# Kernel optimization log

Hardware: AMD Instinct MI355X
Metric: run time of the kernel (lower is better)

The kernel has to match this reference:

```python
import jax, jax.numpy as jnp
import numpy as np

D_H = 128
N_RBF = 16
R_MIN = 0.0
R_MAX = float(np.sqrt(2.0))


def _rbf(r):
    # Gaussian RBF expansion: centers linspace(R_MIN, R_MAX, N_RBF),
    # width = center spacing, exp(-(r-mu)^2 / (2*width^2))
    centers = jnp.linspace(R_MIN, R_MAX, N_RBF, dtype=r.dtype)
    width = (R_MAX - R_MIN) / (N_RBF - 1)
    gamma = 1.0 / (2.0 * width * width)
    return jnp.exp(-gamma * (r[:, None] - centers[None, :]) ** 2)


def setup_inputs() -> dict:
    key = jax.random.key(0)
    ks = jax.random.split(key, 16)
    N, E = 50000, 800000
    h = jax.random.normal(ks[0], (N, D_H), dtype=jnp.float32)
    x = jax.random.uniform(ks[1], (N, 2), dtype=jnp.float32)
    edge_index = jax.random.randint(ks[2], (2, E), 0, N, dtype=jnp.int64)
    edge_weight = jax.random.uniform(ks[3], (E,), dtype=jnp.float32)

    def lin(k, fan_in, fan_out):
        s = 1.0 / np.sqrt(fan_in)
        kw, kb = jax.random.split(k)
        W = jax.random.uniform(kw, (fan_in, fan_out), minval=-s, maxval=s, dtype=jnp.float32)
        b = jax.random.uniform(kb, (fan_out,), minval=-s, maxval=s, dtype=jnp.float32)
        return W, b

    Wm1, bm1 = lin(ks[4], 2 * D_H + N_RBF, D_H)
    Wm2, bm2 = lin(ks[5], D_H, D_H)
    Wh1, bh1 = lin(ks[6], 2 * D_H, D_H)
    Wh2, bh2 = lin(ks[7], D_H, D_H)
    ln_g = jnp.ones((D_H,), dtype=jnp.float32)
    ln_b = jnp.zeros((D_H,), dtype=jnp.float32)
    return {"h": h, "x": x, "edge_index": edge_index, "edge_weight": edge_weight,
            "Wm1": Wm1, "bm1": bm1, "Wm2": Wm2, "bm2": bm2,
            "Wh1": Wh1, "bh1": bh1, "Wh2": Wh2, "bh2": bh2,
            "ln_g": ln_g, "ln_b": ln_b}


def reference(h, x, edge_index, edge_weight, Wm1, bm1, Wm2, bm2, Wh1, bh1, Wh2, bh2, ln_g, ln_b):
    N = h.shape[0]
    src = edge_index[0]
    dst = edge_index[1]
    # per-edge geometry
    dx = x[src, :2] - x[dst, :2]                      # [E,2]
    r = jnp.sqrt(jnp.sum(dx * dx, axis=-1) + 1e-8)    # [E]
    rbf = _rbf(r)                                     # [E,n_rbf]
    # message MLP: Linear -> SiLU -> Linear
    m_in = jnp.concatenate([h[src], h[dst], rbf], axis=-1)  # [E, 2*d_h+n_rbf]
    m = jax.nn.silu(m_in @ Wm1 + bm1) @ Wm2 + bm2            # [E, d_h]
    m = m * edge_weight[:, None]
    # scatter-sum aggregate into destination nodes
    agg = jax.ops.segment_sum(m, dst, num_segments=N)        # [N, d_h]
    # node update MLP
    u_in = jnp.concatenate([h, agg], axis=-1)                # [N, 2*d_h]
    h_up = jax.nn.silu(u_in @ Wh1 + bh1) @ Wh2 + bh2         # [N, d_h]
    # residual + LayerNorm
    z = h + h_up
    mu = jnp.mean(z, axis=-1, keepdims=True)
    var = jnp.var(z, axis=-1, keepdims=True)
    return (z - mu) / jnp.sqrt(var + 1e-5) * ln_g + ln_b
```

## Files before the change

kernel.cpp:

```cpp
#include <hip/hip_runtime.h>
#include <hip/hip_bf16.h>
#include <math.h>

#define DH 128
#define NRBF 16
#define EB 256
#define NTAB 1025
#define SEGCAP 32

typedef unsigned short ushort_t;
typedef __attribute__((ext_vector_type(8))) short short8;
typedef __attribute__((ext_vector_type(4))) float floatx4;

__device__ __forceinline__ float silu_f(float v) {
    return v / (1.f + __expf(-v));
}
__device__ __forceinline__ unsigned pk_bf16(float lo, float hi) {
    __hip_bfloat162 h = __float22bfloat162_rn(make_float2(lo, hi));
    union { __hip_bfloat162 h2; unsigned u; } cv;
    cv.h2 = h;
    return cv.u;
}
__device__ __forceinline__ ushort_t f2bf1(float f) {
    unsigned u = __float_as_uint(f);
    u += 0x7FFFu + ((u >> 16) & 1u);
    return (ushort_t)(u >> 16);
}
__device__ __forceinline__ float bflo(unsigned u) { return __uint_as_float(u << 16); }
__device__ __forceinline__ float bfhi(unsigned u) { return __uint_as_float(u & 0xffff0000u); }
__device__ __forceinline__ float bf2f(ushort_t u) { return __uint_as_float(((unsigned)u) << 16); }

__device__ __forceinline__ int detect64(const int* __restrict__ ei) {
    int z = 0;
#pragma unroll
    for (int i = 0; i < 8; ++i) z |= ei[2 * i + 1];
    return (z == 0) ? 1 : 0;
}
__device__ __forceinline__ int load_dst(const int* ei, int is64, int e, int E) {
    return is64 ? ei[2 * E + 2 * e] : ei[E + e];
}
__device__ __forceinline__ int load_src(const int* ei, int is64, int e, int E) {
    return is64 ? ei[2 * e] : ei[e];
}

__global__ __launch_bounds__(256) void k_hist_prep(
    const int* __restrict__ ei, int* __restrict__ counts, int E,
    const float* __restrict__ Wm1, const float* __restrict__ Wm2,
    const float* __restrict__ Wh1, const float* __restrict__ Wh2,
    ushort_t* __restrict__ Tbf, ushort_t* __restrict__ W2f,
    ushort_t* __restrict__ W1mf, ushort_t* __restrict__ W1hf,
    ushort_t* __restrict__ W2hf, int nb_hist)
{
    const int b = blockIdx.x, tid = threadIdx.x;
    if (b < nb_hist) {
        const int e = b * 256 + tid;
        if (e < E) {
            const int is64 = detect64(ei);
            atomicAdd(&counts[load_dst(ei, is64, e, E)], 1);
        }
        return;
    }
    int b2 = b - nb_hist;
    if (b2 < 257) {
        const int i = b2 * 4 + (tid >> 6);
        if (i < NTAB) {
            const float WIDTH = 0.09428090415820634f;
            const float GAMMA = 56.25f;
            const float DELTA = 1.4142135623730951f / 1024.0f;
            const float r = (float)i * DELTA;
            const int c0 = (tid & 63) * 2;
            float a0 = 0.f, a1 = 0.f;
#pragma unroll
            for (int q = 0; q < NRBF; ++q) {
                const float dr = r - (float)q * WIDTH;
                const float w = __expf(-GAMMA * dr * dr);
                a0 = fmaf(w, Wm1[(256 + q) * DH + c0], a0);
                a1 = fmaf(w, Wm1[(256 + q) * DH + c0 + 1], a1);
            }
            *(unsigned*)(Tbf + (size_t)i * DH + c0) = pk_bf16(a0, a1);
        }
        return;
    }
    b2 -= 257;
    if (b2 < 8) {
        const int u = b2 * 256 + tid;
        const int col = u & 127, kclg = u >> 7;
        const int lg = kclg & 3, kc = kclg >> 2;
        unsigned o[4];
#pragma unroll
        for (int j = 0; j < 2; ++j) {
            o[j]     = pk_bf16(Wm2[(kc * 32 + 4 * lg + 2 * j) * DH + col],
                               Wm2[(kc * 32 + 4 * lg + 2 * j + 1) * DH + col]);
            o[2 + j] = pk_bf16(Wm2[(kc * 32 + 16 + 4 * lg + 2 * j) * DH + col],
                               Wm2[(kc * 32 + 16 + 4 * lg + 2 * j + 1) * DH + col]);
        }
        *(uint4*)(W2f + 8 * u) = make_uint4(o[0], o[1], o[2], o[3]);
        return;
    }
    b2 -= 8;
    if (b2 < 16) {
        const int u = b2 * 256 + tid;
        const int c = u & 255, kclg = u >> 8;
        const int lg = kclg & 3, kc = kclg >> 2;
        const int base = (c < 128) ? 0 : 128;
        const int cc = c & 127;
        unsigned o[4];
#pragma unroll
        for (int j = 0; j < 2; ++j) {
            o[j]     = pk_bf16(Wm1[(base + kc * 32 + 4 * lg + 2 * j) * DH + cc],
                               Wm1[(base + kc * 32 + 4 * lg + 2 * j + 1) * DH + cc]);
            o[2 + j] = pk_bf16(Wm1[(base + kc * 32 + 16 + 4 * lg + 2 * j) * DH + cc],
                               Wm1[(base + kc * 32 + 16 + 4 * lg + 2 * j + 1) * DH + cc]);
        }
        *(uint4*)(W1mf + 8 * u) = make_uint4(o[0], o[1], o[2], o[3]);
        return;
    }
    b2 -= 16;
    if (b2 < 16) {
        const int u = b2 * 256 + tid;
        const int col = u & 127, kclg = u >> 7;
        const int lg = kclg & 3, kc = kclg >> 2;
        unsigned o[4];
#pragma unroll
        for (int j = 0; j < 2; ++j) {
            o[j]     = pk_bf16(Wh1[(kc * 32 + 4 * lg + 2 * j) * DH + col],
                               Wh1[(kc * 32 + 4 * lg + 2 * j + 1) * DH + col]);
            o[2 + j] = pk_bf16(Wh1[(kc * 32 + 16 + 4 * lg + 2 * j) * DH + col],
                               Wh1[(kc * 32 + 16 + 4 * lg + 2 * j + 1) * DH + col]);
        }
        *(uint4*)(W1hf + 8 * u) = make_uint4(o[0], o[1], o[2], o[3]);
        return;
    }
    b2 -= 16;
    {
        const int u = b2 * 256 + tid;
        const int col = u & 127, kclg = u >> 7;
        const int lg = kclg & 3, kc = kclg >> 2;
        unsigned o[4];
#pragma unroll
        for (int j = 0; j < 2; ++j) {
            o[j]     = pk_bf16(Wh2[(kc * 32 + 4 * lg + 2 * j) * DH + col],
                               Wh2[(kc * 32 + 4 * lg + 2 * j + 1) * DH + col]);
            o[2 + j] = pk_bf16(Wh2[(kc * 32 + 16 + 4 * lg + 2 * j) * DH + col],
                               Wh2[(kc * 32 + 16 + 4 * lg + 2 * j + 1) * DH + col]);
        }
        *(uint4*)(W2hf + 8 * u) = make_uint4(o[0], o[1], o[2], o[3]);
    }
}

__global__ __launch_bounds__(1024) void k_scan(const int* __restrict__ counts,
                                               int* __restrict__ cursor, int N) {
    __shared__ int wsum[16];
    __shared__ int sCarry;
    const int tid = threadIdx.x, lane = tid & 63, wid = tid >> 6;
    if (tid == 0) sCarry = 0;
    __syncthreads();
    for (int c0 = 0; c0 < N; c0 += 4096) {
        const int idx = c0 + tid * 4;
        int4 v = make_int4(0, 0, 0, 0);
        if (idx < N) v = *(const int4*)(counts + idx);
        const int t01 = v.x + v.y;
        const int t012 = t01 + v.z;
        const int tot = t012 + v.w;
        int incl = tot;
#pragma unroll
        for (int d = 1; d < 64; d <<= 1) {
            int t = __shfl_up(incl, d, 64);
            if (lane >= d) incl += t;
        }
        if (lane == 63) wsum[wid] = incl;
        __syncthreads();
        if (wid == 0) {
            int s = (lane < 16) ? wsum[lane] : 0;
#pragma unroll
            for (int d = 1; d < 16; d <<= 1) {
                int t = __shfl_up(s, d, 64);
                if (lane >= d) s += t;
            }
            if (lane < 16) wsum[lane] = s;
        }
        __syncthreads();
        const int ex = sCarry + (wid > 0 ? wsum[wid - 1] : 0) + incl - tot;
        if (idx + 3 < N) {
            *(int4*)(cursor + idx) = make_int4(ex, ex + v.x, ex + t01, ex + t012);
        } else if (idx < N) {
            cursor[idx] = ex;
            if (idx + 1 < N) cursor[idx + 1] = ex + v.x;
            if (idx + 2 < N) cursor[idx + 2] = ex + t01;
        }
        __syncthreads();
        if (tid == 0) sCarry += wsum[15];
        __syncthreads();
    }
}

__global__ __launch_bounds__(256) void k_scatter_pre(
    const int* __restrict__ ei, const float* __restrict__ ew, const float* __restrict__ x,
    int* __restrict__ cursor, uint2* __restrict__ spk, int* __restrict__ dstS,
    int E, int pack,
    const float* __restrict__ h, const float* __restrict__ bm1,
    const ushort_t* __restrict__ W1mf,
    ushort_t* __restrict__ Abf, ushort_t* __restrict__ Bbf, int N, int nb_scat)
{
    const int tid = threadIdx.x;

    if ((int)blockIdx.x < nb_scat) {
        const int e = blockIdx.x * 256 + tid;
        if (e < E) {
            const int is64 = detect64(ei);
            const int s = load_src(ei, is64, e, E);
            const int d = load_dst(ei, is64, e, E);
            const int pos = atomicAdd(&cursor[d], 1);
            unsigned x0 = (unsigned)s;
            if (pack) {
                const float2 xs = *(const float2*)(x + 2 * s);
                const float2 xd = *(const float2*)(x + 2 * d);
                const float dxv = xs.x - xd.x, dyv = xs.y - xd.y;
                const float r = sqrtf(dxv * dxv + dyv * dyv + 1e-8f);
                int ti = (int)(r * 724.0773439350246f + 0.5f);
                ti = min(ti, NTAB - 1);
                x0 |= ((unsigned)ti << 16);
            }
            spk[pos] = make_uint2(x0, __float_as_uint(ew[e]));
            dstS[pos] = d;
        }
        return;
    }

    __shared__ __align__(16) ushort_t sIn[64 * DH];
    const int nblk = ((int)blockIdx.x - nb_scat) * 64;

    {
        const int row = tid >> 2, q = tid & 3;
        const int gn = nblk + row;
        const float4* ps = (const float4*)(h + (size_t)gn * DH + 32 * q);
        uint4* rowp = (uint4*)(sIn + row * DH);
        const int swz = row & 7;
#pragma unroll
        for (int i = 0; i < 4; ++i) {
            uint4 o = make_uint4(0, 0, 0, 0);
            if (gn < N) {
                const float4 g0 = ps[2 * i], g1 = ps[2 * i + 1];
                o.x = pk_bf16(g0.x, g0.y); o.y = pk_bf16(g0.z, g0.w);
                o.z = pk_bf16(g1.x, g1.y); o.w = pk_bf16(g1.z, g1.w);
            }
            rowp[(4 * q + i) ^ swz] = o;
        }
    }
    __syncthreads();

    const int lane = tid & 63, wv = tid >> 6;
    const int lr = lane & 15, lg = lane >> 4;
    const int m0l = wv * 16;

    union FragU { unsigned u[4]; short8 s8; };
    floatx4 acc[16];
#pragma unroll
    for (int ni = 0; ni < 16; ++ni) acc[ni] = (floatx4){0.f, 0.f, 0.f, 0.f};

#pragma unroll
    for (int kc = 0; kc < 4; ++kc) {
        const int b1 = 64 * kc + 8 * lg;
        const int b2 = b1 + 32;
        const int row = m0l + lr;
        const char* rbase = (const char*)(sIn + row * DH);
        const int swz = (row & 7) << 4;
        FragU af;
        const uint2 lo = *(const uint2*)(rbase + ((b1 & ~15) ^ swz) + (b1 & 15));
        const uint2 hi = *(const uint2*)(rbase + ((b2 & ~15) ^ swz) + (b2 & 15));
        af.u[0] = lo.x; af.u[1] = lo.y; af.u[2] = hi.x; af.u[3] = hi.y;
        const ushort_t* wbase = W1mf + ((size_t)(kc * 4 + lg) * 256 + lr) * 8;
        __builtin_amdgcn_s_setprio(1);
#pragma unroll
        for (int ni = 0; ni < 16; ++ni) {
            const short8 bf = *(const short8*)(wbase + ni * 128);
            acc[ni] = __builtin_amdgcn_mfma_f32_16x16x32_bf16(af.s8, bf, acc[ni], 0, 0, 0);
        }
        __builtin_amdgcn_s_setprio(0);
    }

    float bm1v[8];
#pragma unroll
    for (int ni = 0; ni < 8; ++ni) bm1v[ni] = bm1[ni * 16 + lr];
#pragma unroll
    for (int r = 0; r < 4; ++r) {
        const int gn = nblk + m0l + 4 * lg + r;
        if (gn < N) {
#pragma unroll
            for (int ni = 0; ni < 8; ++ni)
                Abf[(size_t)gn * DH + ni * 16 + lr] = f2bf1(acc[ni][r] + bm1v[ni]);
#pragma unroll
            for (int ni = 8; ni < 16; ++ni)
                Bbf[(size_t)gn * DH + (ni - 8) * 16 + lr] = f2bf1(acc[ni][r]);
        }
    }
}

__global__ __launch_bounds__(256, 2) void k_edge(
    const float* __restrict__ x, const int* __restrict__ ei, const float* __restrict__ ew,
    const uint2* __restrict__ spk, const int* __restrict__ dstS,
    const ushort_t* __restrict__ W2f, const float* __restrict__ bm2,
    const ushort_t* __restrict__ Abf, const ushort_t* __restrict__ Bbf,
    const ushort_t* __restrict__ Tbf, float* __restrict__ agg,
    int sorted, int pack, int N, int E)
{
    __shared__ __align__(16) ushort_t sHid[4][16 * DH];
    __shared__ __align__(16) float ldsAgg[SEGCAP][DH];
    __shared__ int   sSrc[EB];
    __shared__ int   sDst[EB];
    __shared__ int   sLid[EB];
    __shared__ int   sTi[EB];
    __shared__ float sEw[EB];
    __shared__ int   sSegStart[SEGCAP];
    __shared__ int   sNseg;
    __shared__ int   sWtot[4];

    const int tid  = threadIdx.x;
    const int lane = tid & 63;
    const int wv   = tid >> 6;
    const int lr   = lane & 15;
    const int lg   = lane >> 4;
    const int e4   = lane >> 2;
    const int q    = lane & 3;
    const int wbase = wv * 64;

    const int nwg = gridDim.x;
    const int xcd = blockIdx.x & 7;
    const int cidx = blockIdx.x >> 3;
    const int qch = nwg >> 3, rch = nwg & 7;
    const int bid = (xcd < rch) ? (xcd * (qch + 1) + cidx)
                                : (rch * (qch + 1) + (xcd - rch) * qch + cidx);
    const int e0 = bid * EB;

    const int fast = sorted && pack;

    union FragU { unsigned u[4]; short8 s8; };

    FragU bfr[4][8];
#pragma unroll
    for (int kc = 0; kc < 4; ++kc)
#pragma unroll
        for (int ni = 0; ni < 8; ++ni)
            *(uint4*)bfr[kc][ni].u =
                *(const uint4*)(W2f + ((size_t)(kc * 4 + lg) * 128 + ni * 16 + lr) * 8);

    {
        const float4 z = make_float4(0.f, 0.f, 0.f, 0.f);
        float4* za = (float4*)&ldsAgg[0][0];
#pragma unroll
        for (int i = 0; i < 4; ++i) za[tid + 256 * i] = z;
    }

    {
        const int slot = e0 + tid;
        int s = 0, d = 0, ti = 0;
        float w = 0.f;
        if (slot < E) {
            if (sorted) {
                const uint2 v = spk[slot];
                d = dstS[slot];
                w = __uint_as_float(v.y);
                if (pack) { s = (int)(v.x & 0xFFFFu); ti = (int)(v.x >> 16); }
                else {
                    s = (int)v.x;
                    const float2 xs = *(const float2*)(x + 2 * s);
                    const float2 xd = *(const float2*)(x + 2 * d);
                    const float dxv = xs.x - xd.x, dyv = xs.y - xd.y;
                    const float r = sqrtf(dxv * dxv + dyv * dyv + 1e-8f);
                    ti = min((int)(r * 724.0773439350246f + 0.5f), NTAB - 1);
                }
            } else {
                const int is64 = detect64(ei);
                s = load_src(ei, is64, slot, E);
                d = load_dst(ei, is64, slot, E);
                w = ew[slot];
                const float2 xs = *(const float2*)(x + 2 * s);
                const float2 xd = *(const float2*)(x + 2 * d);
                const float dxv = xs.x - xd.x, dyv = xs.y - xd.y;
                const float r = sqrtf(dxv * dxv + dyv * dyv + 1e-8f);
                ti = min((int)(r * 724.0773439350246f + 0.5f), NTAB - 1);
            }
        } else {
            d = sorted ? dstS[E - 1] : load_dst(ei, detect64(ei), E - 1, E);
        }
        sSrc[tid] = s; sDst[tid] = d; sEw[tid] = w; sTi[tid] = ti;
    }
    __syncthreads();

    {
        const int bflag = (tid > 0) && (sDst[tid] != sDst[tid - 1]);
        int incl = bflag;
#pragma unroll
        for (int dd = 1; dd < 64; dd <<= 1) {
            int t = __shfl_up(incl, dd, 64);
            if (lane >= dd) incl += t;
        }
        if (lane == 63) sWtot[wv] = incl;
        __syncthreads();
        int off = 0;
#pragma unroll
        for (int wq = 0; wq < 3; ++wq)
            if (wq < wv) off += sWtot[wq];
        incl += off;
        sLid[tid] = incl;
        if ((bflag || tid == 0) && incl < SEGCAP) sSegStart[incl] = tid;
        if (tid == EB - 1) sNseg = incl + 1;
    }
    __syncthreads();

    float bc8[8];
#pragma unroll
    for (int ni = 0; ni < 8; ++ni) bc8[ni] = bm2[ni * 16 + lr];

    ushort_t* slice = &sHid[wv][0];
    floatx4 acc[8];

#pragma unroll
    for (int st = 0; st < 4; ++st) {
        const int sb = wbase + st * 16;

        const int le = sb + e4;
        const int s  = sSrc[le];
        const int d  = sDst[le];
        const int ti = sTi[le];
        const uint4* pA = (const uint4*)(Abf + (size_t)s * DH + 32 * q);
        const uint4* pB = (const uint4*)(Bbf + (size_t)d * DH + 32 * q);
        const uint4* pT = (const uint4*)(Tbf + (size_t)ti * DH + 32 * q);
        uint4 av[4], bv[4], tv[4];
#pragma unroll
        for (int i = 0; i < 4; ++i) { av[i] = pA[i]; bv[i] = pB[i]; tv[i] = pT[i]; }

        {
            uint4* rowp = (uint4*)(slice + e4 * DH);
            const int swzw = e4 & 7;
#pragma unroll
            for (int i = 0; i < 4; ++i) {
                const uint4 a = av[i]; const uint4 b = bv[i]; const uint4 t = tv[i];
                const float v0 = bflo(a.x) + bflo(b.x) + bflo(t.x);
                const float v1 = bfhi(a.x) + bfhi(b.x) + bfhi(t.x);
                const float v2 = bflo(a.y) + bflo(b.y) + bflo(t.y);
                const float v3 = bfhi(a.y) + bfhi(b.y) + bfhi(t.y);
                const float v4 = bflo(a.z) + bflo(b.z) + bflo(t.z);
                const float v5 = bfhi(a.z) + bfhi(b.z) + bfhi(t.z);
                const float v6 = bflo(a.w) + bflo(b.w) + bflo(t.w);
                const float v7 = bfhi(a.w) + bfhi(b.w) + bfhi(t.w);
                uint4 pk;
                pk.x = pk_bf16(silu_f(v0), silu_f(v1));
                pk.y = pk_bf16(silu_f(v2), silu_f(v3));
                pk.z = pk_bf16(silu_f(v4), silu_f(v5));
                pk.w = pk_bf16(silu_f(v6), silu_f(v7));
                rowp[(4 * q + i) ^ swzw] = pk;
            }
        }

#pragma unroll
        for (int ni = 0; ni < 8; ++ni) acc[ni] = (floatx4){0.f, 0.f, 0.f, 0.f};
#pragma unroll
        for (int kc = 0; kc < 4; ++kc) {
            const int bo1 = 64 * kc + 8 * lg;
            const int bo2 = bo1 + 32;
            const char* rbase = (const char*)(slice + lr * DH);
            const int swzf = (lr & 7) << 4;
            FragU af;
            const uint2 lo = *(const uint2*)(rbase + ((bo1 & ~15) ^ swzf) + (bo1 & 15));
            const uint2 hi = *(const uint2*)(rbase + ((bo2 & ~15) ^ swzf) + (bo2 & 15));
            af.u[0] = lo.x; af.u[1] = lo.y; af.u[2] = hi.x; af.u[3] = hi.y;
            __builtin_amdgcn_s_setprio(1);
#pragma unroll
            for (int ni = 0; ni < 8; ++ni)
                acc[ni] = __builtin_amdgcn_mfma_f32_16x16x32_bf16(af.s8, bfr[kc][ni].s8, acc[ni], 0, 0, 0);
            __builtin_amdgcn_s_setprio(0);
        }

        {
            const int sbg = sb + 4 * lg;
            int lid4[4]; float ew4[4];
#pragma unroll
            for (int r = 0; r < 4; ++r) { lid4[r] = sLid[sbg + r]; ew4[r] = sEw[sbg + r]; }
#pragma unroll
            for (int ni = 0; ni < 8; ++ni) {
                const int col = ni * 16 + lr;
                const float bc = bc8[ni];
                int cur = lid4[0], curSlot = sbg;
                float avv = (acc[ni][0] + bc) * ew4[0];
#pragma unroll
                for (int r = 1; r < 4; ++r) {
                    const int l2 = lid4[r];
                    const float v = (acc[ni][r] + bc) * ew4[r];
                    if (l2 == cur) avv += v;
                    else {
                        if (cur < SEGCAP) atomicAdd(&ldsAgg[cur][col], avv);
                        else atomicAdd(agg + (size_t)sDst[curSlot] * DH + col, avv);
                        cur = l2; curSlot = sbg + r; avv = v;
                    }
                }
                if (cur < SEGCAP) atomicAdd(&ldsAgg[cur][col], avv);
                else atomicAdd(agg + (size_t)sDst[curSlot] * DH + col, avv);
            }
        }
    }

    __syncthreads();

    const int ns = sNseg;
    const int gmax = (ns < SEGCAP) ? ns : SEGCAP;
    for (int idx = tid; idx < (gmax << 7); idx += 256) {
        const int g = idx >> 7, col = idx & 127;
        const float v = ldsAgg[g][col];
        const int dst = sDst[sSegStart[g]];
        float* p = agg + (size_t)dst * DH + col;
        if (sorted && g > 0 && g < ns - 1) *p = v;
        else atomicAdd(p, v);
    }
}

__global__ __launch_bounds__(256) void k_node(
    const float* __restrict__ h, const float* __restrict__ agg,
    const ushort_t* __restrict__ W1hf, const float* __restrict__ bh1,
    const ushort_t* __restrict__ W2hf, const float* __restrict__ bh2,
    const float* __restrict__ ln_g, const float* __restrict__ ln_b,
    float* __restrict__ out, int N)
{
    __shared__ __align__(16) ushort_t sIn[64 * 256];
    __shared__ __align__(16) ushort_t sHid[64 * DH];
    const int tid = threadIdx.x;
    const int nblk = blockIdx.x * 64;

    {
        const int row = tid >> 2, q = tid & 3;
        const int gn = nblk + row;
        const float4* ps = (q < 2) ? (const float4*)(h + (size_t)gn * DH + 64 * q)
                                   : (const float4*)(agg + (size_t)gn * DH + 64 * (q - 2));
        uint4* rowp = (uint4*)(sIn + row * 256);
        const int swz = row & 7;
#pragma unroll
        for (int i = 0; i < 8; ++i) {
            uint4 o = make_uint4(0, 0, 0, 0);
            if (gn < N) {
                const float4 g0 = ps[2 * i], g1 = ps[2 * i + 1];
                o.x = pk_bf16(g0.x, g0.y); o.y = pk_bf16(g0.z, g0.w);
                o.z = pk_bf16(g1.x, g1.y); o.w = pk_bf16(g1.z, g1.w);
            }
            rowp[(8 * q + i) ^ swz] = o;
        }
    }
    __syncthreads();

    const int lane = tid & 63, wv = tid >> 6;
    const int lr = lane & 15, lg = lane >> 4;
    const int m0l = wv * 16;

    union FragU { unsigned u[4]; short8 s8; };

    floatx4 acc[8];
#pragma unroll
    for (int ni = 0; ni < 8; ++ni) acc[ni] = (floatx4){0.f, 0.f, 0.f, 0.f};

#pragma unroll
    for (int kc = 0; kc < 8; ++kc) {
        const int b1 = 64 * kc + 8 * lg;
        const int b2 = b1 + 32;
        const int row = m0l + lr;
        const char* rbase = (const char*)(sIn + row * 256);
        const int swz = (row & 7) << 4;
        FragU af;
        const uint2 lo = *(const uint2*)(rbase + ((b1 & ~15) ^ swz) + (b1 & 15));
        const uint2 hi = *(const uint2*)(rbase + ((b2 & ~15) ^ swz) + (b2 & 15));
        af.u[0] = lo.x; af.u[1] = lo.y; af.u[2] = hi.x; af.u[3] = hi.y;
        const ushort_t* wbase = W1hf + ((size_t)(kc * 4 + lg) * 128 + lr) * 8;
        __builtin_amdgcn_s_setprio(1);
#pragma unroll
        for (int ni = 0; ni < 8; ++ni) {
            const short8 bf = *(const short8*)(wbase + ni * 128);
            acc[ni] = __builtin_amdgcn_mfma_f32_16x16x32_bf16(af.s8, bf, acc[ni], 0, 0, 0);
        }
        __builtin_amdgcn_s_setprio(0);
    }

    {
        float bh1v[8];
#pragma unroll
        for (int ni = 0; ni < 8; ++ni) bh1v[ni] = bh1[ni * 16 + lr];
#pragma unroll
        for (int r = 0; r < 4; ++r) {
            const int row = m0l + 4 * lg + r;
            const int swz = row & 7;
            ushort_t* rp = sHid + row * DH;
#pragma unroll
            for (int ni = 0; ni < 8; ++ni) {
                const int col = ni * 16 + lr;
                rp[(((col >> 3) ^ swz) << 3) + (col & 7)] =
                    f2bf1(silu_f(acc[ni][r] + bh1v[ni]));
            }
        }
    }

    floatx4 acc2[8];
#pragma unroll
    for (int ni = 0; ni < 8; ++ni) acc2[ni] = (floatx4){0.f, 0.f, 0.f, 0.f};

#pragma unroll
    for (int kc = 0; kc < 4; ++kc) {
        const int b1 = 64 * kc + 8 * lg;
        const int b2 = b1 + 32;
        const int row = m0l + lr;
        const char* rbase = (const char*)(sHid + row * DH);
        const int swz = (row & 7) << 4;
        FragU af;
        const uint2 lo = *(const uint2*)(rbase + ((b1 & ~15) ^ swz) + (b1 & 15));
        const uint2 hi = *(const uint2*)(rbase + ((b2 & ~15) ^ swz) + (b2 & 15));
        af.u[0] = lo.x; af.u[1] = lo.y; af.u[2] = hi.x; af.u[3] = hi.y;
        const ushort_t* wbase = W2hf + ((size_t)(kc * 4 + lg) * 128 + lr) * 8;
        __builtin_amdgcn_s_setprio(1);
#pragma unroll
        for (int ni = 0; ni < 8; ++ni) {
            const short8 bf = *(const short8*)(wbase + ni * 128);
            acc2[ni] = __builtin_amdgcn_mfma_f32_16x16x32_bf16(af.s8, bf, acc2[ni], 0, 0, 0);
        }
        __builtin_amdgcn_s_setprio(0);
    }

    float gv[8], bv[8], b2v[8];
#pragma unroll
    for (int ni = 0; ni < 8; ++ni) {
        const int col = ni * 16 + lr;
        gv[ni] = ln_g[col]; bv[ni] = ln_b[col]; b2v[ni] = bh2[col];
    }
#pragma unroll
    for (int r = 0; r < 4; ++r) {
        const int row = m0l + 4 * lg + r;
        const int gn = nblk + row;
        const int swz = row & 7;
        float z[8];
        float s1 = 0.f, s2 = 0.f;
#pragma unroll
        for (int ni = 0; ni < 8; ++ni) {
            const int col = ni * 16 + lr;
            const float hv = bf2f(sIn[row * 256 + (((col >> 3) ^ swz) << 3) + (col & 7)]);
            z[ni] = acc2[ni][r] + b2v[ni] + hv;
            s1 += z[ni]; s2 += z[ni] * z[ni];
        }
#pragma unroll
        for (int m = 1; m < 16; m <<= 1) {
            s1 += __shfl_xor(s1, m, 64);
            s2 += __shfl_xor(s2, m, 64);
        }
        const float mean = s1 * (1.f / 128.f);
        const float var = s2 * (1.f / 128.f) - mean * mean;
        const float rstd = rsqrtf(var + 1e-5f);
        if (gn < N) {
#pragma unroll
            for (int ni = 0; ni < 8; ++ni) {
                const int col = ni * 16 + lr;
                out[(size_t)gn * DH + col] = (z[ni] - mean) * rstd * gv[ni] + bv[ni];
            }
        }
    }
}

extern "C" void kernel_launch(void* const* d_in, const int* in_sizes, int n_in,
                              void* d_out, int out_size, void* d_ws, size_t ws_size,
                              hipStream_t stream)
{
    (void)n_in; (void)out_size;
    const float* h   = (const float*)d_in[0];
    const float* x   = (const float*)d_in[1];
    const int*   ei  = (const int*)d_in[2];
    const float* ew  = (const float*)d_in[3];
    const float* Wm1 = (const float*)d_in[4];
    const float* bm1 = (const float*)d_in[5];
    const float* Wm2 = (const float*)d_in[6];
    const float* bm2 = (const float*)d_in[7];
    const float* Wh1 = (const float*)d_in[8];
    const float* bh1 = (const float*)d_in[9];
    const float* Wh2 = (const float*)d_in[10];
    const float* bh2 = (const float*)d_in[11];
    const float* lng = (const float*)d_in[12];
    const float* lnb = (const float*)d_in[13];
    float* out = (float*)d_out;

    const int N = in_sizes[0] / DH;
    const int E = in_sizes[3];

    float*    agg  = (float*)d_ws;
    ushort_t* Abf  = (ushort_t*)(agg + (size_t)N * DH);
    ushort_t* Bbf  = Abf + (size_t)N * DH;
    ushort_t* W2f  = Bbf + (size_t)N * DH;
    ushort_t* Tbf  = W2f + 16384;
    ushort_t* W1mf = Tbf + (size_t)NTAB * DH;
    ushort_t* W1hf = W1mf + 32768;
    ushort_t* W2hf = W1hf + 32768;
    int*   counts  = (int*)(W2hf + 16384);
    int*   cursor  = counts + N;
    uint2* spk     = (uint2*)(cursor + N);
    int*   dstS    = (int*)(spk + E);

    const size_t mand = (size_t)N * DH * 4 + (size_t)N * DH * 4
                      + ((size_t)16384 + (size_t)NTAB * DH + 32768 + 32768 + 16384) * 2;
    const size_t need = mand + (size_t)(2 * N) * 4 + (size_t)E * 12 + 64;
    const int use_sort = (ws_size >= need) ? 1 : 0;
    const int pack = use_sort && (N <= 65535);

    const int nb_hist = use_sort ? (E + 255) / 256 : 0;
    const int nb_prep = 257 + 8 + 16 + 16 + 8;
    const int nb_scat = nb_hist;
    const int nb_pre  = (N + 63) / 64;

    hipMemsetAsync(agg, 0, (size_t)N * DH * sizeof(float), stream);
    if (use_sort)
        hipMemsetAsync(counts, 0, (size_t)N * sizeof(int), stream);
    k_hist_prep<<<nb_hist + nb_prep, 256, 0, stream>>>(ei, counts, E, Wm1, Wm2, Wh1, Wh2,
                                                       Tbf, W2f, W1mf, W1hf, W2hf, nb_hist);
    if (use_sort)
        k_scan<<<1, 1024, 0, stream>>>(counts, cursor, N);
    k_scatter_pre<<<nb_scat + nb_pre, 256, 0, stream>>>(ei, ew, x, cursor, spk, dstS, E, pack,
                                                        h, bm1, W1mf, Abf, Bbf, N, nb_scat);
    k_edge<<<(E + EB - 1) / EB, 256, 0, stream>>>(x, ei, ew, spk, dstS,
                                                  W2f, bm2, Abf, Bbf, Tbf, agg,
                                                  use_sort, pack, N, E);
    k_node<<<(N + 63) / 64, 256, 0, stream>>>(h, agg, W1hf, bh1, W2hf, bh2, lng, lnb, out, N);
}
```

Measured before the change: 396.9 us.

## Prefetch all source-row gathers up front and stream W2 fragments from memory

The edge kernel now issues the Abf gathers for all four subtiles at the start and pins them in registers. This is meant to overlap gather latency with compute. To pay for those registers, it stops holding the W2 B-fragments in VGPRs and reloads them from global/L2 inside each MFMA loop. The sorted edge record is packed into one 16-byte uint4 that includes dst, replacing two separate arrays, and counts is placed next to agg so a single memset clears both. This trades higher L2 traffic for W2 and extra bytes per edge record against better latency hiding and fewer launches.

```diff
diff --git a/kernel.cpp b/kernel.cpp
--- a/kernel.cpp
+++ b/kernel.cpp
@@ -42,6 +42,8 @@
 __device__ __forceinline__ int load_src(const int* ei, int is64, int e, int E) {
     return is64 ? ei[2 * e] : ei[e];
 }
+
+#define PIN(u4) asm volatile("" :: "v"(u4.x), "v"(u4.y), "v"(u4.z), "v"(u4.w))
 
 __global__ __launch_bounds__(256) void k_hist_prep(
     const int* __restrict__ ei, int* __restrict__ counts, int E,
@@ -196,7 +198,7 @@
 
 __global__ __launch_bounds__(256) void k_scatter_pre(
     const int* __restrict__ ei, const float* __restrict__ ew, const float* __restrict__ x,
-    int* __restrict__ cursor, uint2* __restrict__ spk, int* __restrict__ dstS,
+    int* __restrict__ cursor, uint4* __restrict__ epk,
     int E, int pack,
     const float* __restrict__ h, const float* __restrict__ bm1,
     const ushort_t* __restrict__ W1mf,
@@ -221,8 +223,7 @@
                 ti = min(ti, NTAB - 1);
                 x0 |= ((unsigned)ti << 16);
             }
-            spk[pos] = make_uint2(x0, __float_as_uint(ew[e]));
-            dstS[pos] = d;
+            epk[pos] = make_uint4(x0, __float_as_uint(ew[e]), (unsigned)d, 0u);
         }
         return;
     }
@@ -298,7 +299,7 @@
 
 __global__ __launch_bounds__(256, 2) void k_edge(
     const float* __restrict__ x, const int* __restrict__ ei, const float* __restrict__ ew,
-    const uint2* __restrict__ spk, const int* __restrict__ dstS,
+    const uint4* __restrict__ epk,
     const ushort_t* __restrict__ W2f, const float* __restrict__ bm2,
     const ushort_t* __restrict__ Abf, const ushort_t* __restrict__ Bbf,
     const ushort_t* __restrict__ Tbf, float* __restrict__ agg,
@@ -332,18 +333,6 @@
                                 : (rch * (qch + 1) + (xcd - rch) * qch + cidx);
     const int e0 = bid * EB;
 
-    const int fast = sorted && pack;
-
-    union FragU { unsigned u[4]; short8 s8; };
-
-    FragU bfr[4][8];
-#pragma unroll
-    for (int kc = 0; kc < 4; ++kc)
-#pragma unroll
-        for (int ni = 0; ni < 8; ++ni)
-            *(uint4*)bfr[kc][ni].u =
-                *(const uint4*)(W2f + ((size_t)(kc * 4 + lg) * 128 + ni * 16 + lr) * 8);
-
     {
         const float4 z = make_float4(0.f, 0.f, 0.f, 0.f);
         float4* za = (float4*)&ldsAgg[0][0];
@@ -357,9 +346,9 @@
         float w = 0.f;
         if (slot < E) {
             if (sorted) {
-                const uint2 v = spk[slot];
-                d = dstS[slot];
+                const uint4 v = epk[slot];
                 w = __uint_as_float(v.y);
+                d = (int)v.z;
                 if (pack) { s = (int)(v.x & 0xFFFFu); ti = (int)(v.x >> 16); }
                 else {
                     s = (int)v.x;
@@ -381,7 +370,7 @@
                 ti = min((int)(r * 724.0773439350246f + 0.5f), NTAB - 1);
             }
         } else {
-            d = sorted ? dstS[E - 1] : load_dst(ei, detect64(ei), E - 1, E);
+            d = sorted ? (int)epk[E - 1].z : load_dst(ei, detect64(ei), E - 1, E);
         }
         sSrc[tid] = s; sDst[tid] = d; sEw[tid] = w; sTi[tid] = ti;
     }
@@ -408,97 +397,125 @@
     }
     __syncthreads();
 
+    uint4 pa0[4], pa1[4], pa2[4], pa3[4];
+    {
+        const uint4* p0 = (const uint4*)(Abf + (size_t)sSrc[wbase +  0 + e4] * DH + 32 * q);
+        const uint4* p1 = (const uint4*)(Abf + (size_t)sSrc[wbase + 16 + e4] * DH + 32 * q);
+        const uint4* p2 = (const uint4*)(Abf + (size_t)sSrc[wbase + 32 + e4] * DH + 32 * q);
+        const uint4* p3 = (const uint4*)(Abf + (size_t)sSrc[wbase + 48 + e4] * DH + 32 * q);
+#pragma unroll
+        for (int i = 0; i < 4; ++i) pa0[i] = p0[i];
+#pragma unroll
+        for (int i = 0; i < 4; ++i) pa1[i] = p1[i];
+#pragma unroll
+        for (int i = 0; i < 4; ++i) pa2[i] = p2[i];
+#pragma unroll
+        for (int i = 0; i < 4; ++i) pa3[i] = p3[i];
+#pragma unroll
+        for (int i = 0; i < 4; ++i) PIN(pa0[i]);
+#pragma unroll
+        for (int i = 0; i < 4; ++i) PIN(pa1[i]);
+#pragma unroll
+        for (int i = 0; i < 4; ++i) PIN(pa2[i]);
+#pragma unroll
+        for (int i = 0; i < 4; ++i) PIN(pa3[i]);
+    }
+
     float bc8[8];
 #pragma unroll
     for (int ni = 0; ni < 8; ++ni) bc8[ni] = bm2[ni * 16 + lr];
 
+    union FragU { unsigned u[4]; short8 s8; };
     ushort_t* slice = &sHid[wv][0];
     floatx4 acc[8];
 
-#pragma unroll
-    for (int st = 0; st < 4; ++st) {
-        const int sb = wbase + st * 16;
-
-        const int le = sb + e4;
-        const int s  = sSrc[le];
-        const int d  = sDst[le];
-        const int ti = sTi[le];
-        const uint4* pA = (const uint4*)(Abf + (size_t)s * DH + 32 * q);
-        const uint4* pB = (const uint4*)(Bbf + (size_t)d * DH + 32 * q);
-        const uint4* pT = (const uint4*)(Tbf + (size_t)ti * DH + 32 * q);
-        uint4 av[4], bv[4], tv[4];
-#pragma unroll
-        for (int i = 0; i < 4; ++i) { av[i] = pA[i]; bv[i] = pB[i]; tv[i] = pT[i]; }
-
-        {
-            uint4* rowp = (uint4*)(slice + e4 * DH);
-            const int swzw = e4 & 7;
-#pragma unroll
-            for (int i = 0; i < 4; ++i) {
-                const uint4 a = av[i]; const uint4 b = bv[i]; const uint4 t = tv[i];
-                const float v0 = bflo(a.x) + bflo(b.x) + bflo(t.x);
-                const float v1 = bfhi(a.x) + bfhi(b.x) + bfhi(t.x);
-                const float v2 = bflo(a.y) + bflo(b.y) + bflo(t.y);
-                const float v3 = bfhi(a.y) + bfhi(b.y) + bfhi(t.y);
-                const float v4 = bflo(a.z) + bflo(b.z) + bflo(t.z);
-                const float v5 = bfhi(a.z) + bfhi(b.z) + bfhi(t.z);
-                const float v6 = bflo(a.w) + bflo(b.w) + bflo(t.w);
-                const float v7 = bfhi(a.w) + bfhi(b.w) + bfhi(t.w);
-                uint4 pk;
-                pk.x = pk_bf16(silu_f(v0), silu_f(v1));
-                pk.y = pk_bf16(silu_f(v2), silu_f(v3));
-                pk.z = pk_bf16(silu_f(v4), silu_f(v5));
-                pk.w = pk_bf16(silu_f(v6), silu_f(v7));
-                rowp[(4 * q + i) ^ swzw] = pk;
-            }
-        }
-
-#pragma unroll
-        for (int ni = 0; ni < 8; ++ni) acc[ni] = (floatx4){0.f, 0.f, 0.f, 0.f};
-#pragma unroll
-        for (int kc = 0; kc < 4; ++kc) {
-            const int bo1 = 64 * kc + 8 * lg;
-            const int bo2 = bo1 + 32;
-            const char* rbase = (const char*)(slice + lr * DH);
-            const int swzf = (lr & 7) << 4;
-            FragU af;
-            const uint2 lo = *(const uint2*)(rbase + ((bo1 & ~15) ^ swzf) + (bo1 & 15));
-            const uint2 hi = *(const uint2*)(rbase + ((bo2 & ~15) ^ swzf) + (bo2 & 15));
-            af.u[0] = lo.x; af.u[1] = lo.y; af.u[2] = hi.x; af.u[3] = hi.y;
-            __builtin_amdgcn_s_setprio(1);
-#pragma unroll
-            for (int ni = 0; ni < 8; ++ni)
-                acc[ni] = __builtin_amdgcn_mfma_f32_16x16x32_bf16(af.s8, bfr[kc][ni].s8, acc[ni], 0, 0, 0);
-            __builtin_amdgcn_s_setprio(0);
-        }
-
-        {
-            const int sbg = sb + 4 * lg;
-            int lid4[4]; float ew4[4];
-#pragma unroll
-            for (int r = 0; r < 4; ++r) { lid4[r] = sLid[sbg + r]; ew4[r] = sEw[sbg + r]; }
-#pragma unroll
-            for (int ni = 0; ni < 8; ++ni) {
-                const int col = ni * 16 + lr;
-                const float bc = bc8[ni];
-                int cur = lid4[0], curSlot = sbg;
-                float avv = (acc[ni][0] + bc) * ew4[0];
-#pragma unroll
-                for (int r = 1; r < 4; ++r) {
-                    const int l2 = lid4[r];
-                    const float v = (acc[ni][r] + bc) * ew4[r];
-                    if (l2 == cur) avv += v;
-                    else {
-                        if (cur < SEGCAP) atomicAdd(&ldsAgg[cur][col], avv);
-                        else atomicAdd(agg + (size_t)sDst[curSlot] * DH + col, avv);
-                        cur = l2; curSlot = sbg + r; avv = v;
-                    }
-                }
-                if (cur < SEGCAP) atomicAdd(&ldsAgg[cur][col], avv);
-                else atomicAdd(agg + (size_t)sDst[curSlot] * DH + col, avv);
-            }
-        }
-    }
+#define SUBTILE(ST, PA)                                                         \
+    {                                                                           \
+        const int sb = wbase + (ST) * 16;                                       \
+        const int le = sb + e4;                                                 \
+        const int dS = sDst[le];                                                \
+        const int tiS = sTi[le];                                                \
+        const uint4* pB = (const uint4*)(Bbf + (size_t)dS * DH + 32 * q);       \
+        const uint4* pT = (const uint4*)(Tbf + (size_t)tiS * DH + 32 * q);      \
+        uint4 bv[4], tv[4];                                                     \
+        _Pragma("unroll")                                                       \
+        for (int i = 0; i < 4; ++i) { bv[i] = pB[i]; tv[i] = pT[i]; }           \
+        {                                                                       \
+            uint4* rowp = (uint4*)(slice + e4 * DH);                            \
+            const int swzw = e4 & 7;                                            \
+            _Pragma("unroll")                                                   \
+            for (int i = 0; i < 4; ++i) {                                       \
+                const uint4 a = PA[i]; const uint4 b = bv[i]; const uint4 t = tv[i]; \
+                const float v0 = bflo(a.x) + bflo(b.x) + bflo(t.x);             \
+                const float v1 = bfhi(a.x) + bfhi(b.x) + bfhi(t.x);             \
+                const float v2 = bflo(a.y) + bflo(b.y) + bflo(t.y);             \
+                const float v3 = bfhi(a.y) + bfhi(b.y) + bfhi(t.y);             \
+                const float v4 = bflo(a.z) + bflo(b.z) + bflo(t.z);             \
+                const float v5 = bfhi(a.z) + bfhi(b.z) + bfhi(t.z);             \
+                const float v6 = bflo(a.w) + bflo(b.w) + bflo(t.w);             \
+                const float v7 = bfhi(a.w) + bfhi(b.w) + bfhi(t.w);             \
+                uint4 pk;                                                       \
+                pk.x = pk_bf16(silu_f(v0), silu_f(v1));                         \
+                pk.y = pk_bf16(silu_f(v2), silu_f(v3));                         \
+                pk.z = pk_bf16(silu_f(v4), silu_f(v5));                         \
+                pk.w = pk_bf16(silu_f(v6), silu_f(v7));                         \
+                rowp[(4 * q + i) ^ swzw] = pk;                                  \
+            }                                                                   \
+        }                                                                       \
+        _Pragma("unroll")                                                       \
+        for (int ni = 0; ni < 8; ++ni) acc[ni] = (floatx4){0.f, 0.f, 0.f, 0.f}; \
+        _Pragma("unroll")                                                       \
+        for (int kc = 0; kc < 4; ++kc) {                                        \
+            const int bo1 = 64 * kc + 8 * lg;                                   \
+            const int bo2 = bo1 + 32;                                           \
+            const char* rbase = (const char*)(slice + lr * DH);                 \
+            const int swzf = (lr & 7) << 4;                                     \
+            FragU af;                                                           \
+            const uint2 lo = *(const uint2*)(rbase + ((bo1 & ~15) ^ swzf) + (bo1 & 15)); \
+            const uint2 hi = *(const uint2*)(rbase + ((bo2 & ~15) ^ swzf) + (bo2 & 15)); \
+            af.u[0] = lo.x; af.u[1] = lo.y; af.u[2] = hi.x; af.u[3] = hi.y;     \
+            const ushort_t* wb2 = W2f + ((size_t)(kc * 4 + lg) * 128 + lr) * 8; \
+            __builtin_amdgcn_s_setprio(1);                                      \
+            _Pragma("unroll")                                                   \
+            for (int ni = 0; ni < 8; ++ni) {                                    \
+                const short8 bf = *(const short8*)(wb2 + ni * 128);             \
+                acc[ni] = __builtin_amdgcn_mfma_f32_16x16x32_bf16(af.s8, bf, acc[ni], 0, 0, 0); \
+            }                                                                   \
+            __builtin_amdgcn_s_setprio(0);                                      \
+        }                                                                       \
+        {                                                                       \
+            const int sbg = sb + 4 * lg;                                        \
+            int lid4[4]; float ew4[4];                                          \
+            _Pragma("unroll")                                                   \
+            for (int r = 0; r < 4; ++r) { lid4[r] = sLid[sbg + r]; ew4[r] = sEw[sbg + r]; } \
+            _Pragma("unroll")                                                   \
+            for (int ni = 0; ni < 8; ++ni) {                                    \
+                const int col = ni * 16 + lr;                                   \
+                const float bc = bc8[ni];                                       \
+                int cur = lid4[0], curSlot = sbg;                               \
+                float avv = (acc[ni][0] + bc) * ew4[0];                         \
+                _Pragma("unroll")                                               \
+                for (int r = 1; r < 4; ++r) {                                   \
+                    const int l2 = lid4[r];                                     \
+                    const float v = (acc[ni][r] + bc) * ew4[r];                 \
+                    if (l2 == cur) avv += v;                                    \
+                    else {                                                      \
+                        if (cur < SEGCAP) atomicAdd(&ldsAgg[cur][col], avv);    \
+                        else atomicAdd(agg + (size_t)sDst[curSlot] * DH + col, avv); \
+                        cur = l2; curSlot = sbg + r; avv = v;                   \
+                    }                                                           \
+                }                                                               \
+                if (cur < SEGCAP) atomicAdd(&ldsAgg[cur][col], avv);            \
+                else atomicAdd(agg + (size_t)sDst[curSlot] * DH + col, avv);    \
+            }                                                                   \
+        }                                                                       \
+    }
+
+    SUBTILE(0, pa0);
+    SUBTILE(1, pa1);
+    SUBTILE(2, pa2);
+    SUBTILE(3, pa3);
+#undef SUBTILE
 
     __syncthreads();
 
@@ -683,21 +700,18 @@
     const int E = in_sizes[3];
 
     float*    agg  = (float*)d_ws;
-    ushort_t* Abf  = (ushort_t*)(agg + (size_t)N * DH);
+    int*   counts  = (int*)(agg + (size_t)N * DH);
+    int*   cursor  = counts + N;
+    ushort_t* Abf  = (ushort_t*)((((uintptr_t)(cursor + N)) + 15) & ~(uintptr_t)15);
     ushort_t* Bbf  = Abf + (size_t)N * DH;
     ushort_t* W2f  = Bbf + (size_t)N * DH;
     ushort_t* Tbf  = W2f + 16384;
     ushort_t* W1mf = Tbf + (size_t)NTAB * DH;
     ushort_t* W1hf = W1mf + 32768;
     ushort_t* W2hf = W1hf + 32768;
-    int*   counts  = (int*)(W2hf + 16384);
-    int*   cursor  = counts + N;
-    uint2* spk     = (uint2*)(cursor + N);
-    int*   dstS    = (int*)(spk + E);
-
-    const size_t mand = (size_t)N * DH * 4 + (size_t)N * DH * 4
-                      + ((size_t)16384 + (size_t)NTAB * DH + 32768 + 32768 + 16384) * 2;
-    const size_t need = mand + (size_t)(2 * N) * 4 + (size_t)E * 12 + 64;
+    uint4* epk     = (uint4*)((((uintptr_t)(W2hf + 16384)) + 15) & ~(uintptr_t)15);
+
+    const size_t need = ((char*)(epk + E)) - ((char*)d_ws);
     const int use_sort = (ws_size >= need) ? 1 : 0;
     const int pack = use_sort && (N <= 65535);
 
@@ -706,16 +720,14 @@
     const int nb_scat = nb_hist;
     const int nb_pre  = (N + 63) / 64;
 
-    hipMemsetAsync(agg, 0, (size_t)N * DH * sizeof(float), stream);
-    if (use_sort)
-        hipMemsetAsync(counts, 0, (size_t)N * sizeof(int), stream);
+    hipMemsetAsync(agg, 0, (size_t)N * DH * sizeof(float) + (use_sort ? (size_t)N * 4 : 0), stream);
     k_hist_prep<<<nb_hist + nb_prep, 256, 0, stream>>>(ei, counts, E, Wm1, Wm2, Wh1, Wh2,
                                                        Tbf, W2f, W1mf, W1hf, W2hf, nb_hist);
     if (use_sort)
         k_scan<<<1, 1024, 0, stream>>>(counts, cursor, N);
-    k_scatter_pre<<<nb_scat + nb_pre, 256, 0, stream>>>(ei, ew, x, cursor, spk, dstS, E, pack,
+    k_scatter_pre<<<nb_scat + nb_pre, 256, 0, stream>>>(ei, ew, x, cursor, epk, E, pack,
                                                         h, bm1, W1mf, Abf, Bbf, N, nb_scat);
-    k_edge<<<(E + EB - 1) / EB, 256, 0, stream>>>(x, ei, ew, spk, dstS,
+    k_edge<<<(E + EB - 1) / EB, 256, 0, stream>>>(x, ei, ew, epk,
                                                   W2f, bm2, Abf, Bbf, Tbf, agg,
                                                   use_sort, pack, N, E);
     k_node<<<(N + 63) / 64, 256, 0, stream>>>(h, agg, W1hf, bh1, W2hf, bh2, lng, lnb, out, N);
```

Result: slower. 428.4 us (+7.9%).

## Stream W2 fragments from memory to raise edge-kernel occupancy; pack edge records

Applied to the files above, without the earlier changes.

The edge kernel no longer holds the full Wm2 bf16 fragment set (32 uint4 per lane) in registers. It reloads each B fragment from global/L2 inside the MFMA loop, and the launch bound is raised from 2 to 4 waves-per-SIMD occupancy so more waves can hide gather latency. The sorted edge record becomes one 16-byte uint4 (src/ti, weight, dst) in place of separate uint2 and int arrays, and the counts buffer is placed next to agg so a single memset clears both. The cost is repeated weight-fragment loads through the cache in the inner loop, plus 4 extra bytes per edge of scatter traffic.

```diff
diff --git a/kernel.cpp b/kernel.cpp
--- a/kernel.cpp
+++ b/kernel.cpp
@@ -196,7 +196,7 @@
 
 __global__ __launch_bounds__(256) void k_scatter_pre(
     const int* __restrict__ ei, const float* __restrict__ ew, const float* __restrict__ x,
-    int* __restrict__ cursor, uint2* __restrict__ spk, int* __restrict__ dstS,
+    int* __restrict__ cursor, uint4* __restrict__ epk,
     int E, int pack,
     const float* __restrict__ h, const float* __restrict__ bm1,
     const ushort_t* __restrict__ W1mf,
@@ -221,8 +221,7 @@
                 ti = min(ti, NTAB - 1);
                 x0 |= ((unsigned)ti << 16);
             }
-            spk[pos] = make_uint2(x0, __float_as_uint(ew[e]));
-            dstS[pos] = d;
+            epk[pos] = make_uint4(x0, __float_as_uint(ew[e]), (unsigned)d, 0u);
         }
         return;
     }
@@ -296,9 +295,9 @@
     }
 }
 
-__global__ __launch_bounds__(256, 2) void k_edge(
+__global__ __launch_bounds__(256, 4) void k_edge(
     const float* __restrict__ x, const int* __restrict__ ei, const float* __restrict__ ew,
-    const uint2* __restrict__ spk, const int* __restrict__ dstS,
+    const uint4* __restrict__ epk,
     const ushort_t* __restrict__ W2f, const float* __restrict__ bm2,
     const ushort_t* __restrict__ Abf, const ushort_t* __restrict__ Bbf,
     const ushort_t* __restrict__ Tbf, float* __restrict__ agg,
@@ -332,18 +331,6 @@
                                 : (rch * (qch + 1) + (xcd - rch) * qch + cidx);
     const int e0 = bid * EB;
 
-    const int fast = sorted && pack;
-
-    union FragU { unsigned u[4]; short8 s8; };
-
-    FragU bfr[4][8];
-#pragma unroll
-    for (int kc = 0; kc < 4; ++kc)
-#pragma unroll
-        for (int ni = 0; ni < 8; ++ni)
-            *(uint4*)bfr[kc][ni].u =
-                *(const uint4*)(W2f + ((size_t)(kc * 4 + lg) * 128 + ni * 16 + lr) * 8);
-
     {
         const float4 z = make_float4(0.f, 0.f, 0.f, 0.f);
         float4* za = (float4*)&ldsAgg[0][0];
@@ -357,9 +344,9 @@
         float w = 0.f;
         if (slot < E) {
             if (sorted) {
-                const uint2 v = spk[slot];
-                d = dstS[slot];
+                const uint4 v = epk[slot];
                 w = __uint_as_float(v.y);
+                d = (int)v.z;
                 if (pack) { s = (int)(v.x & 0xFFFFu); ti = (int)(v.x >> 16); }
                 else {
                     s = (int)v.x;
@@ -381,7 +368,7 @@
                 ti = min((int)(r * 724.0773439350246f + 0.5f), NTAB - 1);
             }
         } else {
-            d = sorted ? dstS[E - 1] : load_dst(ei, detect64(ei), E - 1, E);
+            d = sorted ? (int)epk[E - 1].z : load_dst(ei, detect64(ei), E - 1, E);
         }
         sSrc[tid] = s; sDst[tid] = d; sEw[tid] = w; sTi[tid] = ti;
     }
@@ -412,6 +399,7 @@
 #pragma unroll
     for (int ni = 0; ni < 8; ++ni) bc8[ni] = bm2[ni * 16 + lr];
 
+    union FragU { unsigned u[4]; short8 s8; };
     ushort_t* slice = &sHid[wv][0];
     floatx4 acc[8];
 
@@ -465,10 +453,13 @@
             const uint2 lo = *(const uint2*)(rbase + ((bo1 & ~15) ^ swzf) + (bo1 & 15));
             const uint2 hi = *(const uint2*)(rbase + ((bo2 & ~15) ^ swzf) + (bo2 & 15));
             af.u[0] = lo.x; af.u[1] = lo.y; af.u[2] = hi.x; af.u[3] = hi.y;
+            const ushort_t* wb2 = W2f + ((size_t)(kc * 4 + lg) * 128 + lr) * 8;
             __builtin_amdgcn_s_setprio(1);
 #pragma unroll
-            for (int ni = 0; ni < 8; ++ni)
-                acc[ni] = __builtin_amdgcn_mfma_f32_16x16x32_bf16(af.s8, bfr[kc][ni].s8, acc[ni], 0, 0, 0);
+            for (int ni = 0; ni < 8; ++ni) {
+                const short8 bf = *(const short8*)(wb2 + ni * 128);
+                acc[ni] = __builtin_amdgcn_mfma_f32_16x16x32_bf16(af.s8, bf, acc[ni], 0, 0, 0);
+            }
             __builtin_amdgcn_s_setprio(0);
         }
 
@@ -683,21 +674,18 @@
     const int E = in_sizes[3];
 
     float*    agg  = (float*)d_ws;
-    ushort_t* Abf  = (ushort_t*)(agg + (size_t)N * DH);
+    int*   counts  = (int*)(agg + (size_t)N * DH);
+    int*   cursor  = counts + N;
+    ushort_t* Abf  = (ushort_t*)((((uintptr_t)(cursor + N)) + 15) & ~(uintptr_t)15);
     ushort_t* Bbf  = Abf + (size_t)N * DH;
     ushort_t* W2f  = Bbf + (size_t)N * DH;
     ushort_t* Tbf  = W2f + 16384;
     ushort_t* W1mf = Tbf + (size_t)NTAB * DH;
     ushort_t* W1hf = W1mf + 32768;
     ushort_t* W2hf = W1hf + 32768;
-    int*   counts  = (int*)(W2hf + 16384);
-    int*   cursor  = counts + N;
-    uint2* spk     = (uint2*)(cursor + N);
-    int*   dstS    = (int*)(spk + E);
-
-    const size_t mand = (size_t)N * DH * 4 + (size_t)N * DH * 4
-                      + ((size_t)16384 + (size_t)NTAB * DH + 32768 + 32768 + 16384) * 2;
-    const size_t need = mand + (size_t)(2 * N) * 4 + (size_t)E * 12 + 64;
+    uint4* epk     = (uint4*)((((uintptr_t)(W2hf + 16384)) + 15) & ~(uintptr_t)15);
+
+    const size_t need = ((char*)(epk + E)) - ((char*)d_ws);
     const int use_sort = (ws_size >= need) ? 1 : 0;
     const int pack = use_sort && (N <= 65535);
 
@@ -706,16 +694,14 @@
     const int nb_scat = nb_hist;
     const int nb_pre  = (N + 63) / 64;
 
-    hipMemsetAsync(agg, 0, (size_t)N * DH * sizeof(float), stream);
-    if (use_sort)
-        hipMemsetAsync(counts, 0, (size_t)N * sizeof(int), stream);
+    hipMemsetAsync(agg, 0, (size_t)N * DH * sizeof(float) + (use_sort ? (size_t)N * 4 : 0), stream);
     k_hist_prep<<<nb_hist + nb_prep, 256, 0, stream>>>(ei, counts, E, Wm1, Wm2, Wh1, Wh2,
                                                        Tbf, W2f, W1mf, W1hf, W2hf, nb_hist);
     if (use_sort)
         k_scan<<<1, 1024, 0, stream>>>(counts, cursor, N);
-    k_scatter_pre<<<nb_scat + nb_pre, 256, 0, stream>>>(ei, ew, x, cursor, spk, dstS, E, pack,
+    k_scatter_pre<<<nb_scat + nb_pre, 256, 0, stream>>>(ei, ew, x, cursor, epk, E, pack,
                                                         h, bm1, W1mf, Abf, Bbf, N, nb_scat);
-    k_edge<<<(E + EB - 1) / EB, 256, 0, stream>>>(x, ei, ew, spk, dstS,
+    k_edge<<<(E + EB - 1) / EB, 256, 0, stream>>>(x, ei, ew, epk,
                                                   W2f, bm2, Abf, Bbf, Tbf, agg,
                                                   use_sort, pack, N, E);
     k_node<<<(N + 63) / 64, 256, 0, stream>>>(h, agg, W1hf, bh1, W2hf, bh2, lng, lnb, out, N);
```

After: 403.7 us. No clear change (+1.7%).
